# Optimization experiments

Measured on AMD Instinct MI355X. Metric: run time of the kernel, lower is better.

## Reference

```python
import jax, jax.numpy as jnp
import numpy as np

NUM_HEADS = 16
WINDOW = 256  # window_size: each query i attends to keys [max(0, i-W+1), i]


def setup_inputs() -> dict:
    key = jax.random.key(0)
    k1, k2, k3, k4, k5 = jax.random.split(key, 5)
    B, S, D = 2, 4096, 1024
    scale = 0.02
    return {
        "x": jax.random.normal(k1, (B, S, D), dtype=jnp.float32),
        "wq": jax.random.normal(k2, (D, D), dtype=jnp.float32) * scale,
        "wk": jax.random.normal(k3, (D, D), dtype=jnp.float32) * scale,
        "wv": jax.random.normal(k4, (D, D), dtype=jnp.float32) * scale,
        "wo": jax.random.normal(k5, (D, D), dtype=jnp.float32) * scale,
    }


def _sliding_window_attn(x, wq, wk, wv, wo):
    B, S, D = x.shape
    H, W = NUM_HEADS, WINDOW
    Dh = D // H
    nb = S // W  # number of query blocks (S assumed divisible by W)

    def proj(w):
        # nn.Linear: y = x @ w.T ; -> [B, H, nb, W, Dh]
        y = (x @ w.T).reshape(B, nb, W, H, Dh)
        return y.transpose(0, 3, 1, 2, 4)

    q = proj(wq)
    k = proj(wk)
    v = proj(wv)

    # Each query block j attends to key blocks j-1 and j (banded causal window).
    zpad = jnp.zeros((B, H, 1, W, Dh), dtype=x.dtype)
    kpad = jnp.concatenate([zpad, k], axis=2)  # [B,H,nb+1,W,Dh]
    vpad = jnp.concatenate([zpad, v], axis=2)
    k2 = jnp.concatenate([kpad[:, :, :-1], kpad[:, :, 1:]], axis=3)  # [B,H,nb,2W,Dh]
    v2 = jnp.concatenate([vpad[:, :, :-1], vpad[:, :, 1:]], axis=3)

    scores = jnp.einsum("bhjqd,bhjkd->bhjqk", q, k2) / jnp.sqrt(
        jnp.asarray(Dh, dtype=x.dtype)
    )  # [B,H,nb,W,2W]

    # Mask: query global pos i = j*W + qi; key global pos kp = (j-1)*W + ki.
    # Valid iff i-W+1 <= kp <= i  <=>  qi+1 <= ki <= qi+W ; and kp >= 0.
    qi = jnp.arange(W)[:, None]          # [W,1]
    ki = jnp.arange(2 * W)[None, :]      # [1,2W]
    band = (ki >= qi + 1) & (ki <= qi + W)                      # [W,2W]
    kpos_ok = (jnp.arange(nb)[:, None, None] - 1) * W + ki[None] >= 0  # [nb,1,2W]
    mask = band[None] & kpos_ok          # [nb,W,2W]

    neg = jnp.finfo(scores.dtype).min
    scores = jnp.where(mask[None, None], scores, neg)
    attn = jax.nn.softmax(scores, axis=-1)

    out = jnp.einsum("bhjqk,bhjkd->bhjqd", attn, v2)  # [B,H,nb,W,Dh]
    out = out.transpose(0, 2, 3, 1, 4).reshape(B, S, D)
    return out @ wo.T


def reference(x, wq, wk, wv, wo):
    return _sliding_window_attn(x, wq, wk, wv, wo)
```

## Files before the change

### kernel.cpp

```cpp
#include <hip/hip_runtime.h>

#define S_LEN 4096
#define DMODEL 1024
#define NH 16
#define DH 64
#define WIN 256
#define NQKV 3072

typedef __attribute__((ext_vector_type(8))) short short8;
typedef __attribute__((ext_vector_type(4))) short sh4;
typedef __attribute__((ext_vector_type(4))) float floatx4;

__device__ __forceinline__ ushort f2bf(float f) {
    union { float f; unsigned int i; } x;
    x.f = f;
    unsigned int r = x.i + 0x7FFFu + ((x.i >> 16) & 1u);
    return (ushort)(r >> 16);
}

__global__ __launch_bounds__(256) void cvt_all(const float* __restrict__ x,
                                               const float* __restrict__ wq,
                                               const float* __restrict__ wk,
                                               const float* __restrict__ wv,
                                               const float* __restrict__ wo,
                                               ushort* __restrict__ xb,
                                               ushort* __restrict__ W3b,
                                               ushort* __restrict__ wob,
                                               int nx8, int nw8) {
    int i = blockIdx.x * 256 + threadIdx.x;
    const float* src;
    ushort* dst;
    if (i < nx8) {
        src = x + (size_t)i * 8;            dst = xb + (size_t)i * 8;
    } else {
        int j = i - nx8;
        int which = j / nw8, r = j - which * nw8;
        if (which >= 4) return;
        const float* w4[4] = {wq, wk, wv, wo};
        src = w4[which] + (size_t)r * 8;
        dst = (which == 3 ? wob : W3b + (size_t)which * nw8 * 8) + (size_t)r * 8;
    }
    floatx4 f0 = *(const floatx4*)src;
    floatx4 f1 = *(const floatx4*)(src + 4);
    short8 v;
#pragma unroll
    for (int e = 0; e < 4; ++e) v[e] = (short)f2bf(f0[e]);
#pragma unroll
    for (int e = 0; e < 4; ++e) v[4 + e] = (short)f2bf(f1[e]);
    *(short8*)dst = v;
}

template <bool OUTF32>
__global__ __launch_bounds__(256) void gemm_bf16(const ushort* __restrict__ A,
                                                 const ushort* __restrict__ W,
                                                 void* __restrict__ Cout,
                                                 int M, int N, int K) {
    __shared__ __align__(16) ushort As[128 * 32];
    __shared__ __align__(16) ushort Ws[128 * 32];

    const int tid = threadIdx.x;
    const int w = tid >> 6, l = tid & 63;
    const int bm0 = blockIdx.y * 128, bn0 = blockIdx.x * 128;
    const int wm = (w >> 1) * 64, wn = (w & 1) * 64;
    const int lm = l & 15, quad = l >> 4;

    floatx4 acc[4][4] = {};

    const int row0 = tid >> 2;
    const int gseg = (tid & 3) ^ (row0 & 3) ^ ((row0 >> 2) & 3);

    const ushort* a0 = A + (size_t)(bm0 + row0) * K + gseg * 8;
    const ushort* a1 = A + (size_t)(bm0 + row0 + 64) * K + gseg * 8;
    const ushort* w0 = W + (size_t)(bn0 + row0) * K + gseg * 8;
    const ushort* w1 = W + (size_t)(bn0 + row0 + 64) * K + gseg * 8;

    const int swzl = (lm & 3) ^ ((lm >> 2) & 3);

    for (int k0 = 0; k0 < K; k0 += 32) {
        __builtin_amdgcn_global_load_lds(
            (const __attribute__((address_space(1))) void*)(a0 + k0),
            (__attribute__((address_space(3))) void*)(As + tid * 8), 16, 0, 0);
        __builtin_amdgcn_global_load_lds(
            (const __attribute__((address_space(1))) void*)(a1 + k0),
            (__attribute__((address_space(3))) void*)(As + 2048 + tid * 8), 16, 0, 0);
        __builtin_amdgcn_global_load_lds(
            (const __attribute__((address_space(1))) void*)(w0 + k0),
            (__attribute__((address_space(3))) void*)(Ws + tid * 8), 16, 0, 0);
        __builtin_amdgcn_global_load_lds(
            (const __attribute__((address_space(1))) void*)(w1 + k0),
            (__attribute__((address_space(3))) void*)(Ws + 2048 + tid * 8), 16, 0, 0);
        __syncthreads();

        short8 af[4], wf[4];
        const int sseg = (quad ^ swzl) * 8;
#pragma unroll
        for (int mi = 0; mi < 4; ++mi)
            af[mi] = *(const short8*)&As[(wm + mi * 16 + lm) * 32 + sseg];
#pragma unroll
        for (int ni = 0; ni < 4; ++ni)
            wf[ni] = *(const short8*)&Ws[(wn + ni * 16 + lm) * 32 + sseg];
#pragma unroll
        for (int mi = 0; mi < 4; ++mi)
#pragma unroll
            for (int ni = 0; ni < 4; ++ni)
                acc[mi][ni] = __builtin_amdgcn_mfma_f32_16x16x32_bf16(
                    af[mi], wf[ni], acc[mi][ni], 0, 0, 0);
        __syncthreads();
    }

#pragma unroll
    for (int mi = 0; mi < 4; ++mi) {
#pragma unroll
        for (int ni = 0; ni < 4; ++ni) {
#pragma unroll
            for (int r = 0; r < 4; ++r) {
                int row = bm0 + wm + mi * 16 + quad * 4 + r;
                int col = bn0 + wn + ni * 16 + lm;
                if (OUTF32)
                    ((float*)Cout)[(size_t)row * N + col] = acc[mi][ni][r];
                else
                    ((ushort*)Cout)[(size_t)row * N + col] = f2bf(acc[mi][ni][r]);
            }
        }
    }
}

#define KSP 72
#define VTP 136
#define PSP 40

__global__ __launch_bounds__(256) void swattn_mfma(const ushort* __restrict__ QKV,
                                                   ushort* __restrict__ O) {
    __shared__ __align__(16) ushort Ks[128 * KSP];
    __shared__ __align__(16) ushort Vt[64 * VTP];
    __shared__ __align__(16) ushort Ps[4 * 64 * PSP];
    __shared__ __align__(16) float lW[256];

    const int j = blockIdx.x, h = blockIdx.y, b = blockIdx.z;
    const int tid = threadIdx.x;
    const int w = tid >> 6, l = tid & 63;
    const int quad = l >> 4, lc = l & 15;

    const size_t base = (size_t)b * S_LEN * NQKV + (size_t)h * DH;
    const ushort* Qp = QKV + base;
    const ushort* Kp = QKV + base + DMODEL;
    const ushort* Vp = QKV + base + 2 * DMODEL;

    short8 qf[4][2];
#pragma unroll
    for (int nq = 0; nq < 4; ++nq)
#pragma unroll
        for (int kk = 0; kk < 2; ++kk)
            qf[nq][kk] = *(const short8*)(Qp +
                (size_t)(j * 256 + w * 64 + nq * 16 + lc) * NQKV + kk * 32 + quad * 8);

    floatx4 o[4][4] = {};
    float lsum[4] = {0.f, 0.f, 0.f, 0.f};

    const float sscale = 0.18033688011112042f;
    const float M0 = 2.0f;
    const int qlo = w * 64, qhi = w * 64 + 63;

    for (int c = 0; c < 4; ++c) {
        const int kg0 = (j - 1) * 256 + c * 128;
        if (kg0 < 0) continue;
        __syncthreads();
#pragma unroll
        for (int i = 0; i < 4; ++i) {
            int cc = i * 256 + tid, key = cc >> 3, seg = cc & 7;
            *(short8*)&Ks[key * KSP + seg * 8] =
                *(const short8*)(Kp + (size_t)(kg0 + key) * NQKV + seg * 8);
            short8 vv = *(const short8*)(Vp + (size_t)(kg0 + key) * NQKV + seg * 8);
#pragma unroll
            for (int e = 0; e < 8; ++e)
                Vt[(seg * 8 + e) * VTP + key] = (ushort)vv[e];
        }
        __syncthreads();

        const int krel0 = c * 128 - 256;
#pragma unroll
        for (int g = 0; g < 4; ++g) {
            const int k0 = krel0 + g * 32;
            if (k0 > qhi || k0 + 31 < qlo - 255) continue;

            floatx4 st[2][4];
            const floatx4 zero = {};
#pragma unroll
            for (int kt = 0; kt < 2; ++kt) {
                short8 kf0 = *(const short8*)&Ks[(g * 32 + kt * 16 + lc) * KSP + quad * 8];
                short8 kf1 = *(const short8*)&Ks[(g * 32 + kt * 16 + lc) * KSP + 32 + quad * 8];
#pragma unroll
                for (int nq = 0; nq < 4; ++nq) {
                    st[kt][nq] = __builtin_amdgcn_mfma_f32_16x16x32_bf16(kf0, qf[nq][0], zero, 0, 0, 0);
                    st[kt][nq] = __builtin_amdgcn_mfma_f32_16x16x32_bf16(kf1, qf[nq][1], st[kt][nq], 0, 0, 0);
                }
            }
#pragma unroll
            for (int kt = 0; kt < 2; ++kt)
#pragma unroll
                for (int nq = 0; nq < 4; ++nq) {
                    sh4 pv;
#pragma unroll
                    for (int r = 0; r < 4; ++r) {
                        int krel = k0 + kt * 16 + quad * 4 + r;
                        int qrel = qlo + nq * 16 + lc;
                        bool valid = (krel <= qrel) && (krel + 255 >= qrel);
                        float p = valid ? exp2f(st[kt][nq][r] * sscale - M0) : 0.f;
                        lsum[nq] += p;
                        pv[r] = (short)f2bf(p);
                    }
                    *(sh4*)&Ps[w * 64 * PSP + (nq * 16 + lc) * PSP + kt * 16 + quad * 4] = pv;
                }
            __threadfence_block();

            short8 vf[4];
#pragma unroll
            for (int nd = 0; nd < 4; ++nd)
                vf[nd] = *(const short8*)&Vt[(nd * 16 + lc) * VTP + g * 32 + quad * 8];
#pragma unroll
            for (int mq = 0; mq < 4; ++mq) {
                short8 pf = *(const short8*)&Ps[w * 64 * PSP + (mq * 16 + lc) * PSP + quad * 8];
#pragma unroll
                for (int nd = 0; nd < 4; ++nd)
                    o[mq][nd] = __builtin_amdgcn_mfma_f32_16x16x32_bf16(pf, vf[nd], o[mq][nd], 0, 0, 0);
            }
            __threadfence_block();
        }
    }

#pragma unroll
    for (int nq = 0; nq < 4; ++nq) {
        lsum[nq] += __shfl_xor(lsum[nq], 16);
        lsum[nq] += __shfl_xor(lsum[nq], 32);
    }
    if (l < 16) {
#pragma unroll
        for (int nq = 0; nq < 4; ++nq) lW[w * 64 + nq * 16 + l] = lsum[nq];
    }
    __threadfence_block();
#pragma unroll
    for (int mq = 0; mq < 4; ++mq) {
        floatx4 lv = *(const floatx4*)&lW[w * 64 + mq * 16 + quad * 4];
#pragma unroll
        for (int r = 0; r < 4; ++r) {
            float inv = 1.f / lv[r];
            int token = j * 256 + w * 64 + mq * 16 + quad * 4 + r;
#pragma unroll
            for (int nd = 0; nd < 4; ++nd)
                O[(size_t)b * S_LEN * DMODEL + (size_t)token * DMODEL + h * DH + nd * 16 + lc] =
                    f2bf(o[mq][nd][r] * inv);
        }
    }
}

extern "C" void kernel_launch(void* const* d_in, const int* in_sizes, int n_in,
                              void* d_out, int out_size, void* d_ws, size_t ws_size,
                              hipStream_t stream) {
    const float* x  = (const float*)d_in[0];
    const float* wq = (const float*)d_in[1];
    const float* wk = (const float*)d_in[2];
    const float* wv = (const float*)d_in[3];
    const float* wo = (const float*)d_in[4];
    float* out = (float*)d_out;

    const int D = DMODEL;
    const int M = in_sizes[0] / D;
    const int Bb = M / S_LEN;

    ushort* xb   = (ushort*)d_ws;
    ushort* W3b  = xb + (size_t)M * D;
    ushort* wob  = W3b + (size_t)NQKV * D;
    ushort* QKVb = wob + (size_t)D * D;
    ushort* Ob   = xb;

    const int nx8 = M * D / 8, nw8 = D * D / 8;
    const int ntot = nx8 + 4 * nw8;
    cvt_all<<<dim3((ntot + 255) / 256), dim3(256), 0, stream>>>(
        x, wq, wk, wv, wo, xb, W3b, wob, nx8, nw8);

    gemm_bf16<false><<<dim3(NQKV / 128, M / 128), dim3(256), 0, stream>>>(
        xb, W3b, QKVb, M, NQKV, D);

    swattn_mfma<<<dim3(S_LEN / WIN, NH, Bb), dim3(256), 0, stream>>>(QKVb, Ob);

    gemm_bf16<true><<<dim3(D / 128, M / 128), dim3(256), 0, stream>>>(
        Ob, wob, out, M, D, D);
}
```

Baseline: 246.0 us.

## Widen QKV GEMM tile, drop LDS swizzle, skip masked attention MFMA tiles

Adds a 128x256-tile GEMM used for the QKV projection, which doubles per-block work and reuse of the A tile. It also removes the XOR swizzle from the bf16 GEMM's LDS staging, which may bring back bank conflicts. In attention, 16x16 score and PV sub-tiles that lie entirely outside the band are skipped. The V transpose store layout is also permuted to reduce LDS bank conflicts.

```diff
diff --git a/kernel.cpp b/kernel.cpp
--- a/kernel.cpp
+++ b/kernel.cpp
@@ -66,15 +66,11 @@
 
     floatx4 acc[4][4] = {};
 
-    const int row0 = tid >> 2;
-    const int gseg = (tid & 3) ^ (row0 & 3) ^ ((row0 >> 2) & 3);
-
-    const ushort* a0 = A + (size_t)(bm0 + row0) * K + gseg * 8;
-    const ushort* a1 = A + (size_t)(bm0 + row0 + 64) * K + gseg * 8;
-    const ushort* w0 = W + (size_t)(bn0 + row0) * K + gseg * 8;
-    const ushort* w1 = W + (size_t)(bn0 + row0 + 64) * K + gseg * 8;
-
-    const int swzl = (lm & 3) ^ ((lm >> 2) & 3);
+    const int row0 = tid >> 2, col0 = (tid & 3) * 8;
+    const ushort* a0 = A + (size_t)(bm0 + row0) * K + col0;
+    const ushort* a1 = A + (size_t)(bm0 + row0 + 64) * K + col0;
+    const ushort* w0 = W + (size_t)(bn0 + row0) * K + col0;
+    const ushort* w1 = W + (size_t)(bn0 + row0 + 64) * K + col0;
 
     for (int k0 = 0; k0 < K; k0 += 32) {
         __builtin_amdgcn_global_load_lds(
@@ -92,13 +88,12 @@
         __syncthreads();
 
         short8 af[4], wf[4];
-        const int sseg = (quad ^ swzl) * 8;
 #pragma unroll
         for (int mi = 0; mi < 4; ++mi)
-            af[mi] = *(const short8*)&As[(wm + mi * 16 + lm) * 32 + sseg];
+            af[mi] = *(const short8*)&As[(wm + mi * 16 + lm) * 32 + quad * 8];
 #pragma unroll
         for (int ni = 0; ni < 4; ++ni)
-            wf[ni] = *(const short8*)&Ws[(wn + ni * 16 + lm) * 32 + sseg];
+            wf[ni] = *(const short8*)&Ws[(wn + ni * 16 + lm) * 32 + quad * 8];
 #pragma unroll
         for (int mi = 0; mi < 4; ++mi)
 #pragma unroll
@@ -109,9 +104,9 @@
     }
 
 #pragma unroll
-    for (int mi = 0; mi < 4; ++mi) {
-#pragma unroll
-        for (int ni = 0; ni < 4; ++ni) {
+    for (int mi = 0; mi < 4; ++mi)
+#pragma unroll
+        for (int ni = 0; ni < 4; ++ni)
 #pragma unroll
             for (int r = 0; r < 4; ++r) {
                 int row = bm0 + wm + mi * 16 + quad * 4 + r;
@@ -121,8 +116,82 @@
                 else
                     ((ushort*)Cout)[(size_t)row * N + col] = f2bf(acc[mi][ni][r]);
             }
-        }
-    }
+}
+
+template <bool OUTF32>
+__global__ __launch_bounds__(256, 2) void gemm_wide(const ushort* __restrict__ A,
+                                                    const ushort* __restrict__ W,
+                                                    void* __restrict__ Cout,
+                                                    int M, int N, int K) {
+    __shared__ __align__(16) ushort As[128 * 32];
+    __shared__ __align__(16) ushort Ws[256 * 32];
+
+    const int tid = threadIdx.x;
+    const int w = tid >> 6, l = tid & 63;
+    const int bm0 = blockIdx.y * 128, bn0 = blockIdx.x * 256;
+    const int wm = (w >> 1) * 64, wn = (w & 1) * 128;
+    const int lm = l & 15, quad = l >> 4;
+
+    floatx4 acc[4][8] = {};
+
+    const int row0 = tid >> 2, col0 = (tid & 3) * 8;
+    const ushort* a0 = A + (size_t)(bm0 + row0) * K + col0;
+    const ushort* a1 = A + (size_t)(bm0 + row0 + 64) * K + col0;
+    const ushort* wp0 = W + (size_t)(bn0 + row0) * K + col0;
+    const ushort* wp1 = W + (size_t)(bn0 + row0 + 64) * K + col0;
+    const ushort* wp2 = W + (size_t)(bn0 + row0 + 128) * K + col0;
+    const ushort* wp3 = W + (size_t)(bn0 + row0 + 192) * K + col0;
+
+    for (int k0 = 0; k0 < K; k0 += 32) {
+        __builtin_amdgcn_global_load_lds(
+            (const __attribute__((address_space(1))) void*)(a0 + k0),
+            (__attribute__((address_space(3))) void*)(As + tid * 8), 16, 0, 0);
+        __builtin_amdgcn_global_load_lds(
+            (const __attribute__((address_space(1))) void*)(a1 + k0),
+            (__attribute__((address_space(3))) void*)(As + 2048 + tid * 8), 16, 0, 0);
+        __builtin_amdgcn_global_load_lds(
+            (const __attribute__((address_space(1))) void*)(wp0 + k0),
+            (__attribute__((address_space(3))) void*)(Ws + tid * 8), 16, 0, 0);
+        __builtin_amdgcn_global_load_lds(
+            (const __attribute__((address_space(1))) void*)(wp1 + k0),
+            (__attribute__((address_space(3))) void*)(Ws + 2048 + tid * 8), 16, 0, 0);
+        __builtin_amdgcn_global_load_lds(
+            (const __attribute__((address_space(1))) void*)(wp2 + k0),
+            (__attribute__((address_space(3))) void*)(Ws + 4096 + tid * 8), 16, 0, 0);
+        __builtin_amdgcn_global_load_lds(
+            (const __attribute__((address_space(1))) void*)(wp3 + k0),
+            (__attribute__((address_space(3))) void*)(Ws + 6144 + tid * 8), 16, 0, 0);
+        __syncthreads();
+
+        short8 af[4], wf[8];
+#pragma unroll
+        for (int mi = 0; mi < 4; ++mi)
+            af[mi] = *(const short8*)&As[(wm + mi * 16 + lm) * 32 + quad * 8];
+#pragma unroll
+        for (int ni = 0; ni < 8; ++ni)
+            wf[ni] = *(const short8*)&Ws[(wn + ni * 16 + lm) * 32 + quad * 8];
+#pragma unroll
+        for (int mi = 0; mi < 4; ++mi)
+#pragma unroll
+            for (int ni = 0; ni < 8; ++ni)
+                acc[mi][ni] = __builtin_amdgcn_mfma_f32_16x16x32_bf16(
+                    af[mi], wf[ni], acc[mi][ni], 0, 0, 0);
+        __syncthreads();
+    }
+
+#pragma unroll
+    for (int mi = 0; mi < 4; ++mi)
+#pragma unroll
+        for (int ni = 0; ni < 8; ++ni)
+#pragma unroll
+            for (int r = 0; r < 4; ++r) {
+                int row = bm0 + wm + mi * 16 + quad * 4 + r;
+                int col = bn0 + wn + ni * 16 + lm;
+                if (OUTF32)
+                    ((float*)Cout)[(size_t)row * N + col] = acc[mi][ni][r];
+                else
+                    ((ushort*)Cout)[(size_t)row * N + col] = f2bf(acc[mi][ni][r]);
+            }
 }
 
 #define KSP 72
@@ -173,7 +242,7 @@
             short8 vv = *(const short8*)(Vp + (size_t)(kg0 + key) * NQKV + seg * 8);
 #pragma unroll
             for (int e = 0; e < 8; ++e)
-                Vt[(seg * 8 + e) * VTP + key] = (ushort)vv[e];
+                Vt[(e * 8 + seg) * VTP + key] = (ushort)vv[e];
         }
         __syncthreads();
 
@@ -191,6 +260,11 @@
                 short8 kf1 = *(const short8*)&Ks[(g * 32 + kt * 16 + lc) * KSP + 32 + quad * 8];
 #pragma unroll
                 for (int nq = 0; nq < 4; ++nq) {
+                    int kmin = k0 + kt * 16, qmin = qlo + nq * 16;
+                    if (kmin > qmin + 15 || kmin + 15 + 255 < qmin) {
+                        st[kt][nq] = zero;
+                        continue;
+                    }
                     st[kt][nq] = __builtin_amdgcn_mfma_f32_16x16x32_bf16(kf0, qf[nq][0], zero, 0, 0, 0);
                     st[kt][nq] = __builtin_amdgcn_mfma_f32_16x16x32_bf16(kf1, qf[nq][1], st[kt][nq], 0, 0, 0);
                 }
@@ -200,14 +274,19 @@
 #pragma unroll
                 for (int nq = 0; nq < 4; ++nq) {
                     sh4 pv;
-#pragma unroll
-                    for (int r = 0; r < 4; ++r) {
-                        int krel = k0 + kt * 16 + quad * 4 + r;
-                        int qrel = qlo + nq * 16 + lc;
-                        bool valid = (krel <= qrel) && (krel + 255 >= qrel);
-                        float p = valid ? exp2f(st[kt][nq][r] * sscale - M0) : 0.f;
-                        lsum[nq] += p;
-                        pv[r] = (short)f2bf(p);
+                    int kmin = k0 + kt * 16, qmin = qlo + nq * 16;
+                    if (kmin > qmin + 15 || kmin + 15 + 255 < qmin) {
+                        pv[0] = pv[1] = pv[2] = pv[3] = 0;
+                    } else {
+#pragma unroll
+                        for (int r = 0; r < 4; ++r) {
+                            int krel = kmin + quad * 4 + r;
+                            int qrel = qmin + lc;
+                            bool valid = (krel <= qrel) && (krel + 255 >= qrel);
+                            float p = valid ? exp2f(st[kt][nq][r] * sscale - M0) : 0.f;
+                            lsum[nq] += p;
+                            pv[r] = (short)f2bf(p);
+                        }
                     }
                     *(sh4*)&Ps[w * 64 * PSP + (nq * 16 + lc) * PSP + kt * 16 + quad * 4] = pv;
                 }
@@ -215,10 +294,14 @@
 
             short8 vf[4];
 #pragma unroll
-            for (int nd = 0; nd < 4; ++nd)
-                vf[nd] = *(const short8*)&Vt[(nd * 16 + lc) * VTP + g * 32 + quad * 8];
+            for (int nd = 0; nd < 4; ++nd) {
+                int prow = (lc & 7) * 8 + nd * 2 + (lc >> 3);
+                vf[nd] = *(const short8*)&Vt[prow * VTP + g * 32 + quad * 8];
+            }
 #pragma unroll
             for (int mq = 0; mq < 4; ++mq) {
+                int qmin = qlo + mq * 16;
+                if (k0 > qmin + 15 || k0 + 31 + 255 < qmin) continue;
                 short8 pf = *(const short8*)&Ps[w * 64 * PSP + (mq * 16 + lc) * PSP + quad * 8];
 #pragma unroll
                 for (int nd = 0; nd < 4; ++nd)
@@ -278,7 +361,7 @@
     cvt_all<<<dim3((ntot + 255) / 256), dim3(256), 0, stream>>>(
         x, wq, wk, wv, wo, xb, W3b, wob, nx8, nw8);
 
-    gemm_bf16<false><<<dim3(NQKV / 128, M / 128), dim3(256), 0, stream>>>(
+    gemm_wide<false><<<dim3(NQKV / 256, M / 128), dim3(256), 0, stream>>>(
         xb, W3b, QKVb, M, NQKV, D);
 
     swattn_mfma<<<dim3(S_LEN / WIN, NH, Bb), dim3(256), 0, stream>>>(QKVb, Ob);
```

Result: no change. 246.5 us (+0.2%).
